# Kernel optimization log

Measured on AMD Instinct MI355X. Metric: run time of the kernel, lower is better.

Reference implementation:

```python
import jax, jax.numpy as jnp
import numpy as np

E = 1024
H = 16
D = E // H
EPS = 1e-5


def _layernorm(x, g, b):
    mu = jnp.mean(x, axis=-1, keepdims=True)
    var = jnp.mean(jnp.square(x - mu), axis=-1, keepdims=True)
    return (x - mu) * jax.lax.rsqrt(var + EPS) * g + b


def setup_inputs() -> dict:
    key = jax.random.key(0)
    ks = jax.random.split(key, 12)
    B, T = 2, 2048
    s_e = 1.0 / np.sqrt(E)
    s_f = 1.0 / np.sqrt(4 * E)
    return {
        "x": jax.random.normal(ks[0], (B, T, E), jnp.float32),
        "ln1_g": jnp.ones((E,), jnp.float32),
        "ln1_b": jnp.zeros((E,), jnp.float32),
        "w_qkv": jax.random.normal(ks[1], (E, 3 * E), jnp.float32) * s_e,
        "b_qkv": jnp.zeros((3 * E,), jnp.float32),
        "w_out": jax.random.normal(ks[2], (E, E), jnp.float32) * s_e,
        "b_out": jnp.zeros((E,), jnp.float32),
        "ln2_g": jnp.ones((E,), jnp.float32),
        "ln2_b": jnp.zeros((E,), jnp.float32),
        "w_fc": jax.random.normal(ks[3], (E, 4 * E), jnp.float32) * s_e,
        "b_fc": jnp.zeros((4 * E,), jnp.float32),
        "w_proj": jax.random.normal(ks[4], (4 * E, E), jnp.float32) * s_f,
        "b_proj": jnp.zeros((E,), jnp.float32),
    }


def _attn(h, w_qkv, b_qkv, w_out, b_out):
    B, T, _ = h.shape
    qkv = h @ w_qkv + b_qkv                      # [B,T,3E]
    # torch: view(B,T,H,3*D).chunk(3,-1) -> per-head interleaved q,k,v
    qkv = qkv.reshape(B, T, H, 3, D)
    q = jnp.transpose(qkv[..., 0, :], (0, 2, 1, 3))  # [B,H,T,D]
    k = jnp.transpose(qkv[..., 1, :], (0, 2, 1, 3))
    v = jnp.transpose(qkv[..., 2, :], (0, 2, 1, 3))
    scores = jnp.einsum("bhqd,bhkd->bhqk", q, k) / np.sqrt(D)
    mask = jnp.tril(jnp.ones((T, T), bool))
    scores = jnp.where(mask, scores, -jnp.inf)
    w = jax.nn.softmax(scores, axis=-1)
    out = jnp.einsum("bhqk,bhkd->bhqd", w, v)    # [B,H,T,D]
    out = jnp.transpose(out, (0, 2, 1, 3)).reshape(B, T, E)
    return out @ w_out + b_out


def reference(x, ln1_g, ln1_b, w_qkv, b_qkv, w_out, b_out,
              ln2_g, ln2_b, w_fc, b_fc, w_proj, b_proj):
    x = x + _attn(_layernorm(x, ln1_g, ln1_b), w_qkv, b_qkv, w_out, b_out)
    h = _layernorm(x, ln2_g, ln2_b)
    h = jax.nn.gelu(h @ w_fc + b_fc, approximate=True) @ w_proj + b_proj
    return x + h
```

## Files before the change

### kernel.cpp

```cpp
#include <hip/hip_runtime.h>
#include <hip/hip_bf16.h>


#define T_DIM 2048
#define E_DIM 1024
#define NH 16

using short8 = __attribute__((__ext_vector_type__(8))) short;
using f32x4  = __attribute__((__ext_vector_type__(4))) float;

static __device__ __forceinline__ f32x4 zero4() {
  f32x4 z = {0.f, 0.f, 0.f, 0.f};
  return z;
}

static __device__ __forceinline__ unsigned short f2bfbits(float f) {
  __hip_bfloat16 h = __float2bfloat16(f);
  return *reinterpret_cast<unsigned short*>(&h);
}

static __device__ __forceinline__ float gelu_tanh(float x) {
  float z = 0.7978845608028654f * (x + 0.044715f * x * x * x);
  float e = __expf(2.0f * z);
  float th = 1.0f - 2.0f / (e + 1.0f);
  return 0.5f * x * (1.0f + th);
}

__global__ __launch_bounds__(256) void prep(
    const float* __restrict__ w_qkv, const float* __restrict__ w_out,
    const float* __restrict__ w_fc, const float* __restrict__ w_proj,
    __hip_bfloat16* __restrict__ t_qkv, __hip_bfloat16* __restrict__ t_out,
    __hip_bfloat16* __restrict__ t_fc, __hip_bfloat16* __restrict__ t_proj,
    const float* __restrict__ x, const float* __restrict__ g,
    const float* __restrict__ bb, __hip_bfloat16* __restrict__ ln1o) {
  __shared__ float tl[64][65];
  const int id = blockIdx.x;
  const int t = threadIdx.x;
  if (id < 3072) {
    const float* in;
    __hip_bfloat16* out;
    int K, N, bx, by;
    if (id < 768) {
      in = w_qkv; out = t_qkv; K = 1024; N = 3072; bx = id % 48; by = id / 48;
    } else if (id < 1024) {
      const int i = id - 768;
      in = w_out; out = t_out; K = 1024; N = 1024; bx = i % 16; by = i / 16;
    } else if (id < 2048) {
      const int i = id - 1024;
      in = w_fc; out = t_fc; K = 1024; N = 4096; bx = i % 64; by = i / 64;
    } else {
      const int i = id - 2048;
      in = w_proj; out = t_proj; K = 4096; N = 1024; bx = i % 16; by = i / 16;
    }
    const int n0 = bx * 64, k0 = by * 64;
    const int rr = t >> 4;
    const int cc = (t & 15) * 4;
#pragma unroll
    for (int i = 0; i < 4; ++i) {
      const int row = rr + i * 16;
      const float4 v = *reinterpret_cast<const float4*>(&in[(size_t)(k0 + row) * N + n0 + cc]);
      tl[row][cc] = v.x; tl[row][cc + 1] = v.y; tl[row][cc + 2] = v.z; tl[row][cc + 3] = v.w;
    }
    __syncthreads();
#pragma unroll
    for (int i = 0; i < 4; ++i) {
      const int row = rr + i * 16;
      ushort4 pk;
      pk.x = f2bfbits(tl[cc + 0][row]);
      pk.y = f2bfbits(tl[cc + 1][row]);
      pk.z = f2bfbits(tl[cc + 2][row]);
      pk.w = f2bfbits(tl[cc + 3][row]);
      *reinterpret_cast<ushort4*>(&out[(size_t)(n0 + row) * K + k0 + cc]) = pk;
    }
  } else {
    const int lane = t & 63;
    const int row = (id - 3072) * 4 + (t >> 6);
    const float* xr = x + (size_t)row * E_DIM;
    float4 v[4];
    float s = 0.f, s2 = 0.f;
#pragma unroll
    for (int i = 0; i < 4; ++i) {
      v[i] = *reinterpret_cast<const float4*>(&xr[(i * 64 + lane) * 4]);
      s  += v[i].x + v[i].y + v[i].z + v[i].w;
      s2 += v[i].x * v[i].x + v[i].y * v[i].y + v[i].z * v[i].z + v[i].w * v[i].w;
    }
#pragma unroll
    for (int m = 1; m < 64; m <<= 1) { s += __shfl_xor(s, m); s2 += __shfl_xor(s2, m); }
    const float mu = s * (1.0f / E_DIM);
    const float var = s2 * (1.0f / E_DIM) - mu * mu;
    const float rstd = rsqrtf(var + 1e-5f);
    __hip_bfloat16* orow = ln1o + (size_t)row * E_DIM;
#pragma unroll
    for (int i = 0; i < 4; ++i) {
      const int col = (i * 64 + lane) * 4;
      const float4 gv = *reinterpret_cast<const float4*>(&g[col]);
      const float4 bv = *reinterpret_cast<const float4*>(&bb[col]);
      ushort4 pk;
      pk.x = f2bfbits((v[i].x - mu) * rstd * gv.x + bv.x);
      pk.y = f2bfbits((v[i].y - mu) * rstd * gv.y + bv.y);
      pk.z = f2bfbits((v[i].z - mu) * rstd * gv.z + bv.z);
      pk.w = f2bfbits((v[i].w - mu) * rstd * gv.w + bv.w);
      *reinterpret_cast<ushort4*>(&orow[col]) = pk;
    }
  }
}

__global__ __launch_bounds__(256) void layernorm_bf16(
    const float* __restrict__ x, const float* __restrict__ g, const float* __restrict__ bb,
    __hip_bfloat16* __restrict__ out) {
  const int lane = threadIdx.x & 63;
  const int row = blockIdx.x * 4 + (threadIdx.x >> 6);
  const float* xr = x + (size_t)row * E_DIM;
  float4 v[4];
  float s = 0.f, s2 = 0.f;
#pragma unroll
  for (int i = 0; i < 4; ++i) {
    v[i] = *reinterpret_cast<const float4*>(&xr[(i * 64 + lane) * 4]);
    s  += v[i].x + v[i].y + v[i].z + v[i].w;
    s2 += v[i].x * v[i].x + v[i].y * v[i].y + v[i].z * v[i].z + v[i].w * v[i].w;
  }
#pragma unroll
  for (int m = 1; m < 64; m <<= 1) { s += __shfl_xor(s, m); s2 += __shfl_xor(s2, m); }
  const float mu = s * (1.0f / E_DIM);
  const float var = s2 * (1.0f / E_DIM) - mu * mu;
  const float rstd = rsqrtf(var + 1e-5f);
  __hip_bfloat16* orow = out + (size_t)row * E_DIM;
#pragma unroll
  for (int i = 0; i < 4; ++i) {
    const int col = (i * 64 + lane) * 4;
    const float4 gv = *reinterpret_cast<const float4*>(&g[col]);
    const float4 bv = *reinterpret_cast<const float4*>(&bb[col]);
    ushort4 pk;
    pk.x = f2bfbits((v[i].x - mu) * rstd * gv.x + bv.x);
    pk.y = f2bfbits((v[i].y - mu) * rstd * gv.y + bv.y);
    pk.z = f2bfbits((v[i].z - mu) * rstd * gv.z + bv.z);
    pk.w = f2bfbits((v[i].w - mu) * rstd * gv.w + bv.w);
    *reinterpret_cast<ushort4*>(&orow[col]) = pk;
  }
}

template <int GELU_ACT, int ADD_RES, int OUT_F32, int SCALE_Q>
__global__ __launch_bounds__(256, 2) void gemm_bt(
    const __hip_bfloat16* __restrict__ A, const __hip_bfloat16* __restrict__ Bt,
    const float* __restrict__ bias, const float* __restrict__ res,
    float* __restrict__ outF, __hip_bfloat16* __restrict__ outB,
    int M, int N, int K) {
  __shared__ __hip_bfloat16 sA[2][128 * 32];
  __shared__ __hip_bfloat16 sB[2][128 * 32];
  const int tid = threadIdx.x;
  const int w = tid >> 6, l = tid & 63;
  const int lhi = l >> 4, llo = l & 15;
  const int gx = gridDim.x;
  int wg = blockIdx.y * gx + blockIdx.x;
  const int cpx = (gx * gridDim.y) >> 3;
  wg = (wg & 7) * cpx + (wg >> 3);
  const int m0 = (wg / gx) * 128, n0 = (wg % gx) * 128;
  const int wr = (w >> 1) * 64, wc = (w & 1) * 64;
  f32x4 acc[4][4];
#pragma unroll
  for (int i = 0; i < 4; ++i)
#pragma unroll
    for (int j = 0; j < 4; ++j) acc[i][j] = zero4();

  const int nt = K >> 5;
  const int cswz = (((tid & 3) ^ ((tid >> 2) & 3)) << 3);
  auto stage = [&](int buf, int t) {
    const int k0 = t << 5;
#pragma unroll
    for (int i = 0; i < 2; ++i) {
      const int r = i * 64 + (tid >> 2);
      const int e = i * 2048 + tid * 8;
      __builtin_amdgcn_global_load_lds(
          (const __attribute__((address_space(1))) void*)(A + (size_t)(m0 + r) * K + k0 + cswz),
          (__attribute__((address_space(3))) void*)(&sA[buf][e]), 16, 0, 0);
      __builtin_amdgcn_global_load_lds(
          (const __attribute__((address_space(1))) void*)(Bt + (size_t)(n0 + r) * K + k0 + cswz),
          (__attribute__((address_space(3))) void*)(&sB[buf][e]), 16, 0, 0);
    }
  };

  stage(0, 0);
  for (int t = 0; t < nt; ++t) {
    const int cur = t & 1;
    __syncthreads();
    if (t + 1 < nt) stage(cur ^ 1, t + 1);
    const __hip_bfloat16* pa = sA[cur];
    const __hip_bfloat16* pb = sB[cur];
    short8 af[4], bfr[4];
    const int gsw = (lhi ^ (llo & 3)) << 3;
#pragma unroll
    for (int i = 0; i < 4; ++i) {
      af[i]  = *reinterpret_cast<const short8*>(pa + (wr + i * 16 + llo) * 32 + gsw);
      bfr[i] = *reinterpret_cast<const short8*>(pb + (wc + i * 16 + llo) * 32 + gsw);
    }
#pragma unroll
    for (int mi = 0; mi < 4; ++mi)
#pragma unroll
      for (int ni = 0; ni < 4; ++ni)
        acc[mi][ni] = __builtin_amdgcn_mfma_f32_16x16x32_bf16(af[mi], bfr[ni], acc[mi][ni], 0, 0, 0);
  }

#pragma unroll
  for (int mi = 0; mi < 4; ++mi) {
#pragma unroll
    for (int ni = 0; ni < 4; ++ni) {
      const int row = m0 + wr + mi * 16 + lhi * 4;
      const int col = n0 + wc + ni * 16 + llo;
      const float bc = bias[col];
      float qs = 1.0f;
      if (SCALE_Q) qs = ((col % 192) < 64) ? 0.125f : 1.0f;
#pragma unroll
      for (int j = 0; j < 4; ++j) {
        float v = acc[mi][ni][j] + bc;
        if (SCALE_Q) v *= qs;
        if (GELU_ACT) v = gelu_tanh(v);
        if (ADD_RES) v += res[(size_t)(row + j) * N + col];
        if (OUT_F32) outF[(size_t)(row + j) * N + col] = v;
        else outB[(size_t)(row + j) * N + col] = __float2bfloat16(v);
      }
    }
  }
}

__global__ __launch_bounds__(256) void transpose_v(
    const __hip_bfloat16* __restrict__ qkv, __hip_bfloat16* __restrict__ vt) {
  const int t0 = blockIdx.x * 64, h = blockIdx.y, b = blockIdx.z;
  const size_t rb = (size_t)b * T_DIM;
  const size_t obase = ((size_t)(b * NH + h) * 64) * T_DIM;
  __shared__ unsigned short tl[64][64];
  const int tid = threadIdx.x;
#pragma unroll
  for (int k = 0; k < 2; ++k) {
    const int e = k * 2048 + tid * 8;
    const int tr = e >> 6, dc = e & 63;
    const short8 v =
        *reinterpret_cast<const short8*>(qkv + (rb + t0 + tr) * 3072 + h * 192 + 128 + dc);
    *reinterpret_cast<short8*>(&tl[tr][dc ^ ((tr & 7) << 3)]) = v;
  }
  __syncthreads();
#pragma unroll
  for (int k = 0; k < 2; ++k) {
    const int e = k * 2048 + tid * 8;
    const int dr = e >> 6, tc = e & 63;
    short8 o;
#pragma unroll
    for (int jj = 0; jj < 8; ++jj)
      o[jj] = (short)tl[tc + jj][dr ^ (((tc + jj) & 7) << 3)];
    *reinterpret_cast<short8*>(&vt[obase + (size_t)dr * T_DIM + t0 + tc]) = o;
  }
}

__global__ __launch_bounds__(256) void attn_fwd(
    const __hip_bfloat16* __restrict__ qkv, const __hip_bfloat16* __restrict__ vt,
    __hip_bfloat16* __restrict__ aout) {
  const int hb = blockIdx.x;
  const int h = hb & 15, b = hb >> 4;
  const int tid = threadIdx.x, w = tid >> 6, l = tid & 63;
  const int lhi = l >> 4, llo = l & 15;
  const int pr = w >> 1;
  const int s = w & 1;
  const int p = blockIdx.y * 2 + pr;
  const size_t rb = (size_t)b * T_DIM;
  const size_t vbase = ((size_t)(b * NH + h) * 64) * T_DIM;
  __shared__ __hip_bfloat16 sP[4][32][72];
  __shared__ float mrg[2][64][49];

  short8 onesb;
#pragma unroll
  for (int i = 0; i < 8; ++i) onesb[i] = (short)0x3F80;

#pragma unroll
  for (int half = 0; half < 2; ++half) {
    const int tile = half ? (63 - p) : p;
    const int q0 = tile * 32;
    const int nkv = (tile >> 1) + 1;
    const int base = (tile & 1) << 5;
    const int kt_begin = s ? (nkv >> 1) : 0;
    const int kt_end   = s ? nkv : (nkv >> 1);

    short8 qf[2][2];
#pragma unroll
    for (int mf = 0; mf < 2; ++mf) {
      const __hip_bfloat16* qp =
          qkv + ((rb + q0 + mf * 16 + llo) * 3072 + h * 192 + lhi * 8);
      qf[mf][0] = *reinterpret_cast<const short8*>(qp);
      qf[mf][1] = *reinterpret_cast<const short8*>(qp + 32);
    }
    float mrun[2][4], lrun[2][4];
    f32x4 oacc[2][4];
#pragma unroll
    for (int mf = 0; mf < 2; ++mf)
#pragma unroll
      for (int j = 0; j < 4; ++j) { mrun[mf][j] = -1e30f; lrun[mf][j] = 0.f; }
#pragma unroll
    for (int mf = 0; mf < 2; ++mf)
#pragma unroll
      for (int di = 0; di < 4; ++di) oacc[mf][di] = zero4();

    auto loadK = [&](short8 (&dst)[4][2], int k0) {
#pragma unroll
      for (int ni = 0; ni < 4; ++ni) {
        const __hip_bfloat16* kp =
            qkv + ((rb + k0 + ni * 16 + llo) * 3072 + h * 192 + 64 + lhi * 8);
        dst[ni][0] = *reinterpret_cast<const short8*>(kp);
        dst[ni][1] = *reinterpret_cast<const short8*>(kp + 32);
      }
    };

    auto step = [&](short8 (&cK)[4][2], short8 (&nK)[4][2], int kt) {
      const bool diag = (kt == nkv - 1);
      const bool evendiag = diag && (base == 0);
      f32x4 sc[2][4];
      __builtin_amdgcn_s_setprio(1);
#pragma unroll
      for (int mf = 0; mf < 2; ++mf)
#pragma unroll
        for (int ni = 0; ni < 4; ++ni) {
          sc[mf][ni] = zero4();
          if (!evendiag || ni < 2) {
            sc[mf][ni] =
                __builtin_amdgcn_mfma_f32_16x16x32_bf16(qf[mf][0], cK[ni][0], sc[mf][ni], 0, 0, 0);
            sc[mf][ni] =
                __builtin_amdgcn_mfma_f32_16x16x32_bf16(qf[mf][1], cK[ni][1], sc[mf][ni], 0, 0, 0);
          }
        }
      __builtin_amdgcn_s_setprio(0);
      if (kt + 1 < kt_end) loadK(nK, (kt + 1) * 64);
      short8 vCur[4][2];
#pragma unroll
      for (int di = 0; di < 4; ++di) {
        const __hip_bfloat16* vp =
            vt + (vbase + (size_t)(di * 16 + llo) * T_DIM + kt * 64 + lhi * 8);
        vCur[di][0] = *reinterpret_cast<const short8*>(vp);
        vCur[di][1] = *reinterpret_cast<const short8*>(vp + 32);
      }
      float mx[2][4];
      bool ok = true;
#pragma unroll
      for (int mf = 0; mf < 2; ++mf)
#pragma unroll
        for (int j = 0; j < 4; ++j) {
          const int ql = mf * 16 + lhi * 4 + j;
#pragma unroll
          for (int ni = 0; ni < 4; ++ni) {
            float sval = sc[mf][ni][j];
            if (diag) sval = (ni * 16 + llo <= base + ql) ? sval : -1e30f;
            sc[mf][ni][j] = sval;
          }
          float m = fmaxf(fmaxf(sc[mf][0][j], sc[mf][1][j]),
                          fmaxf(sc[mf][2][j], sc[mf][3][j]));
#pragma unroll
          for (int d = 1; d < 16; d <<= 1) m = fmaxf(m, __shfl_xor(m, d));
          mx[mf][j] = m;
          ok = ok && (m <= mrun[mf][j] + 8.0f);
        }
      float corr[2][4];
      if (__all((int)ok)) {
#pragma unroll
        for (int mf = 0; mf < 2; ++mf)
#pragma unroll
          for (int j = 0; j < 4; ++j) {
            corr[mf][j] = 1.0f;
#pragma unroll
            for (int ni = 0; ni < 4; ++ni)
              sP[w][mf * 16 + lhi * 4 + j][ni * 16 + llo] =
                  __float2bfloat16(__expf(sc[mf][ni][j] - mrun[mf][j]));
          }
      } else {
#pragma unroll
        for (int mf = 0; mf < 2; ++mf)
#pragma unroll
          for (int j = 0; j < 4; ++j) {
            const float mnew = fmaxf(mrun[mf][j], mx[mf][j]);
            const float c = __expf(mrun[mf][j] - mnew);
            mrun[mf][j] = mnew;
            corr[mf][j] = c;
#pragma unroll
            for (int ni = 0; ni < 4; ++ni)
              sP[w][mf * 16 + lhi * 4 + j][ni * 16 + llo] =
                  __float2bfloat16(__expf(sc[mf][ni][j] - mnew));
#pragma unroll
            for (int di = 0; di < 4; ++di) oacc[mf][di][j] *= c;
          }
      }
      asm volatile("s_waitcnt lgkmcnt(0)" ::: "memory");
      __builtin_amdgcn_s_setprio(1);
#pragma unroll
      for (int mf = 0; mf < 2; ++mf) {
        const short8 pf0 = *reinterpret_cast<const short8*>(&sP[w][mf * 16 + llo][lhi * 8]);
        const short8 pf1 = *reinterpret_cast<const short8*>(&sP[w][mf * 16 + llo][32 + lhi * 8]);
        f32x4 lacc = zero4();
        lacc = __builtin_amdgcn_mfma_f32_16x16x32_bf16(pf0, onesb, lacc, 0, 0, 0);
        if (!evendiag)
          lacc = __builtin_amdgcn_mfma_f32_16x16x32_bf16(pf1, onesb, lacc, 0, 0, 0);
#pragma unroll
        for (int di = 0; di < 4; ++di) {
          oacc[mf][di] =
              __builtin_amdgcn_mfma_f32_16x16x32_bf16(pf0, vCur[di][0], oacc[mf][di], 0, 0, 0);
          if (!evendiag)
            oacc[mf][di] =
                __builtin_amdgcn_mfma_f32_16x16x32_bf16(pf1, vCur[di][1], oacc[mf][di], 0, 0, 0);
        }
#pragma unroll
        for (int j = 0; j < 4; ++j)
          lrun[mf][j] = lrun[mf][j] * corr[mf][j] + lacc[j];
      }
      __builtin_amdgcn_s_setprio(0);
    };

    short8 kA[4][2], kB[4][2];
    if (kt_begin < kt_end) loadK(kA, kt_begin * 64);
    for (int kt = kt_begin; kt < kt_end; ++kt) {
      if ((kt - kt_begin) & 1) step(kB, kA, kt);
      else                     step(kA, kB, kt);
    }

    if (s == 0) {
      float* dst = &mrg[pr][l][0];
#pragma unroll
      for (int mf = 0; mf < 2; ++mf)
#pragma unroll
        for (int di = 0; di < 4; ++di)
#pragma unroll
          for (int j = 0; j < 4; ++j) dst[(mf * 4 + di) * 4 + j] = oacc[mf][di][j];
#pragma unroll
      for (int mf = 0; mf < 2; ++mf)
#pragma unroll
        for (int j = 0; j < 4; ++j) {
          dst[32 + mf * 4 + j] = mrun[mf][j];
          dst[40 + mf * 4 + j] = lrun[mf][j];
        }
    }
    __syncthreads();
    if (s == 1) {
      const float* src = &mrg[pr][l][0];
#pragma unroll
      for (int mf = 0; mf < 2; ++mf)
#pragma unroll
        for (int j = 0; j < 4; ++j) {
          const float m0 = src[32 + mf * 4 + j], l0 = src[40 + mf * 4 + j];
          const float m1 = mrun[mf][j], l1 = lrun[mf][j];
          const float mm = fmaxf(m0, m1);
          const float a0 = __expf(m0 - mm), a1 = __expf(m1 - mm);
          const float linv = 1.0f / (l0 * a0 + l1 * a1);
          const size_t row = rb + q0 + mf * 16 + lhi * 4 + j;
#pragma unroll
          for (int di = 0; di < 4; ++di) {
            const float o = (src[(mf * 4 + di) * 4 + j] * a0 + oacc[mf][di][j] * a1) * linv;
            aout[row * 1024 + h * 64 + di * 16 + llo] = __float2bfloat16(o);
          }
        }
    }
    __syncthreads();
  }
}

extern "C" void kernel_launch(void* const* d_in, const int* in_sizes, int n_in,
                              void* d_out, int out_size, void* d_ws, size_t ws_size,
                              hipStream_t stream) {
  (void)in_sizes; (void)n_in; (void)out_size; (void)ws_size;
  const float* x      = (const float*)d_in[0];
  const float* ln1_g  = (const float*)d_in[1];
  const float* ln1_b  = (const float*)d_in[2];
  const float* w_qkv  = (const float*)d_in[3];
  const float* b_qkv  = (const float*)d_in[4];
  const float* w_out  = (const float*)d_in[5];
  const float* b_out  = (const float*)d_in[6];
  const float* ln2_g  = (const float*)d_in[7];
  const float* ln2_b  = (const float*)d_in[8];
  const float* w_fc   = (const float*)d_in[9];
  const float* b_fc   = (const float*)d_in[10];
  const float* w_proj = (const float*)d_in[11];
  const float* b_proj = (const float*)d_in[12];
  float* out = (float*)d_out;

  const int M = 2 * T_DIM;
  char* wsp = (char*)d_ws;
  size_t off = 0;
  auto carve = [&](size_t bytes) {
    void* p = wsp + off;
    off += (bytes + 255) & ~(size_t)255;
    return p;
  };
  __hip_bfloat16* wt_qkv  = (__hip_bfloat16*)carve((size_t)3072 * 1024 * 2);
  __hip_bfloat16* wt_out  = (__hip_bfloat16*)carve((size_t)1024 * 1024 * 2);
  __hip_bfloat16* wt_fc   = (__hip_bfloat16*)carve((size_t)4096 * 1024 * 2);
  __hip_bfloat16* wt_proj = (__hip_bfloat16*)carve((size_t)1024 * 4096 * 2);
  __hip_bfloat16* ln1o    = (__hip_bfloat16*)carve((size_t)M * 1024 * 2);
  __hip_bfloat16* qkvb    = (__hip_bfloat16*)carve((size_t)M * 3072 * 2);
  __hip_bfloat16* vtb     = (__hip_bfloat16*)carve((size_t)2 * NH * 64 * T_DIM * 2);
  __hip_bfloat16* attnb   = (__hip_bfloat16*)carve((size_t)M * 1024 * 2);
  float*          x2      = (float*)carve((size_t)M * 1024 * 4);
  __hip_bfloat16* h1      = (__hip_bfloat16*)carve((size_t)M * 4096 * 2);
  __hip_bfloat16* ln2o    = ln1o;

  prep<<<4096, 256, 0, stream>>>(w_qkv, w_out, w_fc, w_proj,
                                 wt_qkv, wt_out, wt_fc, wt_proj,
                                 x, ln1_g, ln1_b, ln1o);
  gemm_bt<0, 0, 0, 1><<<dim3(3072 / 128, M / 128), 256, 0, stream>>>(
      ln1o, wt_qkv, b_qkv, nullptr, nullptr, qkvb, M, 3072, 1024);
  transpose_v<<<dim3(T_DIM / 64, NH, 2), 256, 0, stream>>>(qkvb, vtb);
  attn_fwd<<<dim3(32, 16), 256, 0, stream>>>(qkvb, vtb, attnb);
  gemm_bt<0, 1, 1, 0><<<dim3(1024 / 128, M / 128), 256, 0, stream>>>(
      attnb, wt_out, b_out, x, x2, nullptr, M, 1024, 1024);
  layernorm_bf16<<<M / 4, 256, 0, stream>>>(x2, ln2_g, ln2_b, ln2o);
  gemm_bt<1, 0, 0, 0><<<dim3(4096 / 128, M / 128), 256, 0, stream>>>(
      ln2o, wt_fc, b_fc, nullptr, nullptr, h1, M, 4096, 1024);
  gemm_bt<0, 1, 1, 0><<<dim3(1024 / 128, M / 128), 256, 0, stream>>>(
      h1, wt_proj, b_proj, x2, out, nullptr, M, 1024, 4096);
}
```

Before: 319.1 us.

## Raise GEMM occupancy hint and drop lazy-rescale branch in attention softmax

The GEMM launch bound now asks for 3 workgroups per CU instead of 2, which caps registers per thread so more waves can overlap. The attention inner loop drops the lazy-rescale scheme, where the running max was updated only when the new max exceeded it by more than a threshold, and always applies the online-softmax correction. This removes the wave vote and the two-way branch at the cost of an extra exp and accumulator rescale on every tile. The tighter register cap may cause spills in the GEMM.

Result: no change. 314.1 us (-1.6%).

```diff
diff --git a/kernel.cpp b/kernel.cpp
--- a/kernel.cpp
+++ b/kernel.cpp
@@ -140,7 +140,7 @@
 }
 
 template <int GELU_ACT, int ADD_RES, int OUT_F32, int SCALE_Q>
-__global__ __launch_bounds__(256, 2) void gemm_bt(
+__global__ __launch_bounds__(256, 3) void gemm_bt(
     const __hip_bfloat16* __restrict__ A, const __hip_bfloat16* __restrict__ Bt,
     const float* __restrict__ bias, const float* __restrict__ res,
     float* __restrict__ outF, __hip_bfloat16* __restrict__ outB,
@@ -334,55 +334,32 @@
         vCur[di][0] = *reinterpret_cast<const short8*>(vp);
         vCur[di][1] = *reinterpret_cast<const short8*>(vp + 32);
       }
-      float mx[2][4];
-      bool ok = true;
+      float corr[2][4];
 #pragma unroll
       for (int mf = 0; mf < 2; ++mf)
 #pragma unroll
         for (int j = 0; j < 4; ++j) {
           const int ql = mf * 16 + lhi * 4 + j;
+          float sv[4];
 #pragma unroll
           for (int ni = 0; ni < 4; ++ni) {
             float sval = sc[mf][ni][j];
             if (diag) sval = (ni * 16 + llo <= base + ql) ? sval : -1e30f;
-            sc[mf][ni][j] = sval;
+            sv[ni] = sval;
           }
-          float m = fmaxf(fmaxf(sc[mf][0][j], sc[mf][1][j]),
-                          fmaxf(sc[mf][2][j], sc[mf][3][j]));
-#pragma unroll
-          for (int d = 1; d < 16; d <<= 1) m = fmaxf(m, __shfl_xor(m, d));
-          mx[mf][j] = m;
-          ok = ok && (m <= mrun[mf][j] + 8.0f);
+          float mx = fmaxf(fmaxf(sv[0], sv[1]), fmaxf(sv[2], sv[3]));
+#pragma unroll
+          for (int d = 1; d < 16; d <<= 1) mx = fmaxf(mx, __shfl_xor(mx, d));
+          const float mnew = fmaxf(mrun[mf][j], mx);
+          const float c = __expf(mrun[mf][j] - mnew);
+          mrun[mf][j] = mnew;
+          corr[mf][j] = c;
+#pragma unroll
+          for (int ni = 0; ni < 4; ++ni)
+            sP[w][mf * 16 + lhi * 4 + j][ni * 16 + llo] = __float2bfloat16(__expf(sv[ni] - mnew));
+#pragma unroll
+          for (int di = 0; di < 4; ++di) oacc[mf][di][j] *= c;
         }
-      float corr[2][4];
-      if (__all((int)ok)) {
-#pragma unroll
-        for (int mf = 0; mf < 2; ++mf)
-#pragma unroll
-          for (int j = 0; j < 4; ++j) {
-            corr[mf][j] = 1.0f;
-#pragma unroll
-            for (int ni = 0; ni < 4; ++ni)
-              sP[w][mf * 16 + lhi * 4 + j][ni * 16 + llo] =
-                  __float2bfloat16(__expf(sc[mf][ni][j] - mrun[mf][j]));
-          }
-      } else {
-#pragma unroll
-        for (int mf = 0; mf < 2; ++mf)
-#pragma unroll
-          for (int j = 0; j < 4; ++j) {
-            const float mnew = fmaxf(mrun[mf][j], mx[mf][j]);
-            const float c = __expf(mrun[mf][j] - mnew);
-            mrun[mf][j] = mnew;
-            corr[mf][j] = c;
-#pragma unroll
-            for (int ni = 0; ni < 4; ++ni)
-              sP[w][mf * 16 + lhi * 4 + j][ni * 16 + llo] =
-                  __float2bfloat16(__expf(sc[mf][ni][j] - mnew));
-#pragma unroll
-            for (int di = 0; di < 4; ++di) oacc[mf][di][j] *= c;
-          }
-      }
       asm volatile("s_waitcnt lgkmcnt(0)" ::: "memory");
       __builtin_amdgcn_s_setprio(1);
 #pragma unroll
```
